# Performance work log

Hardware: AMD Instinct MI355X
Metric: run time of the kernel (lower is better)

## Reference

```python
import jax, jax.numpy as jnp
import numpy as np

B, T, C = 4, 2048, 1024
N_HEAD = 16
HEAD_DIM = C // N_HEAD
SCALE = 1.0 / np.sqrt(HEAD_DIM).astype(np.float32)


def setup_inputs() -> dict:
    key = jax.random.key(0)
    k1, k2, k3 = jax.random.split(key, 3)
    x = jax.random.normal(k1, (B, T, C), dtype=jnp.float32)
    # torch Linear weights: [out_features, in_features], scaled init
    w_qkv = jax.random.normal(k2, (3 * C, C), dtype=jnp.float32) * (1.0 / np.sqrt(C))
    w_out = jax.random.normal(k3, (C, C), dtype=jnp.float32) * (1.0 / np.sqrt(C))
    b_out = jnp.zeros((C,), dtype=jnp.float32)
    return {"x": x, "w_qkv": w_qkv, "w_out": w_out, "b_out": b_out}


def reference(x, w_qkv, w_out, b_out):
    Bsz, Tlen, Cdim = x.shape
    qkv = jnp.einsum('btc,oc->bto', x, w_qkv)  # [B,T,3C]
    q, k, v = jnp.split(qkv, 3, axis=-1)
    # [B,H,T,D]
    def heads(t):
        return t.reshape(Bsz, Tlen, N_HEAD, HEAD_DIM).transpose(0, 2, 1, 3)
    q, k, v = heads(q), heads(k), heads(v)
    att = jnp.einsum('bhqd,bhkd->bhqk', q, k) * SCALE  # [B,H,T,T]
    causal = jnp.tril(jnp.ones((Tlen, Tlen), dtype=bool))
    att = jnp.where(causal[None, None], att, -jnp.inf)
    att = jax.nn.softmax(att, axis=-1)
    out = jnp.einsum('bhqk,bhkd->bhqd', att, v)
    out = out.transpose(0, 2, 1, 3).reshape(Bsz, Tlen, Cdim)
    out = jnp.einsum('btc,oc->bto', out, w_out) + b_out
    return out
```

## Files before the change

kernel.cpp:

```cpp
#include <hip/hip_runtime.h>
#include <stdint.h>


typedef __attribute__((ext_vector_type(8))) short bf16x8;
typedef __attribute__((ext_vector_type(4))) float f32x4;

#define EXP2F(x) __builtin_amdgcn_exp2f(x)
#define SL2E 0.18033688011112042f
#define FIXED_M 15.0f

__device__ __forceinline__ short f2bf(float f) {
  union { float f; unsigned u; } c; c.f = f;
  unsigned u = c.u;
  unsigned r = (u + 0x7fffu + ((u >> 16) & 1u)) >> 16;
  return (short)(unsigned short)r;
}

__device__ __forceinline__ short f2bf_trunc(float f) {
  union { float f; unsigned u; } c; c.f = f;
  return (short)(unsigned short)(c.u >> 16);
}

__device__ __forceinline__ void llds16(const short* g, short* l) {
  __builtin_amdgcn_global_load_lds(
      (const __attribute__((address_space(1))) unsigned int*)g,
      (__attribute__((address_space(3))) unsigned int*)l, 16, 0, 0);
}

__global__ __launch_bounds__(256) void cast_f32_to_bf16(
    const float* __restrict__ src, short* __restrict__ dst, int n4) {
  int i = blockIdx.x * 256 + threadIdx.x;
  if (i >= n4) return;
  float4 f = ((const float4*)src)[i];
  short4 o;
  o.x = f2bf(f.x); o.y = f2bf(f.y); o.z = f2bf(f.z); o.w = f2bf(f.w);
  ((short4*)dst)[i] = o;
}

__global__ __launch_bounds__(256) void transpose_v(
    const short* __restrict__ V, short* __restrict__ Vt) {
  const int T = 2048;
  __shared__ short lT[64 * 72];
  const int tid = threadIdx.x;
  const int t0 = blockIdx.x * 64;
  const int bh = blockIdx.y;
  const size_t ib = (size_t)bh * T * 64;
  const size_t ob = (size_t)bh * 64 * T;
#pragma unroll
  for (int call = 0; call < 2; ++call) {
    const int c = call * 256 + tid;
    bf16x8 vv = *(const bf16x8*)(V + ib + (size_t)(t0 + (c >> 3)) * 64 + (c & 7) * 8);
#pragma unroll
    for (int jj = 0; jj < 8; ++jj)
      lT[((c & 7) * 8 + jj) * 72 + (c >> 3)] = vv[jj];
  }
  __syncthreads();
#pragma unroll
  for (int call = 0; call < 2; ++call) {
    const int c = call * 256 + tid;
    bf16x8 o = *(const bf16x8*)&lT[(c >> 3) * 72 + (c & 7) * 8];
    *(bf16x8*)(Vt + ob + (size_t)(c >> 3) * T + t0 + (c & 7) * 8) = o;
  }
}

__global__ __launch_bounds__(256) void gemm_qkv(
    const short* __restrict__ A, const short* __restrict__ Bw,
    short* __restrict__ Qo, short* __restrict__ Ko, short* __restrict__ Vo) {
  const int K = 1024;
  __shared__ short lA[128 * 32];
  __shared__ short lB[128 * 32];
  __shared__ short lC[128 * 132];
  const int tid = threadIdx.x;
  const int lane = tid & 63;
  const int wave = tid >> 6;
  const int m0 = blockIdx.y * 128;
  const int n0 = blockIdx.x * 128;
  const int wm = (wave >> 1) * 64;
  const int wn = (wave & 1) * 64;
  const int mrow = lane & 15;
  const int kq = lane >> 4;

  f32x4 acc[4][4];
#pragma unroll
  for (int i = 0; i < 4; ++i)
#pragma unroll
    for (int j = 0; j < 4; ++j) acc[i][j] = (f32x4){0.f, 0.f, 0.f, 0.f};

  for (int k0 = 0; k0 < K; k0 += 32) {
#pragma unroll
    for (int call = 0; call < 2; ++call) {
      const int cb = call * 256 + wave * 64;
      const int c = cb + lane;
      llds16(A + (size_t)(m0 + (c >> 2)) * K + k0 + (c & 3) * 8, &lA[cb * 8]);
      llds16(Bw + (size_t)(n0 + (c >> 2)) * K + k0 + (c & 3) * 8, &lB[cb * 8]);
    }
    __syncthreads();
    bf16x8 af[4], bfr[4];
#pragma unroll
    for (int i = 0; i < 4; ++i)
      af[i] = *(const bf16x8*)&lA[(wm + i * 16 + mrow) * 32 + kq * 8];
#pragma unroll
    for (int j = 0; j < 4; ++j)
      bfr[j] = *(const bf16x8*)&lB[(wn + j * 16 + mrow) * 32 + kq * 8];
#pragma unroll
    for (int i = 0; i < 4; ++i)
#pragma unroll
      for (int j = 0; j < 4; ++j)
        acc[i][j] = __builtin_amdgcn_mfma_f32_16x16x32_bf16(af[i], bfr[j], acc[i][j], 0, 0, 0);
    __syncthreads();
  }

#pragma unroll
  for (int i = 0; i < 4; ++i) {
    const int row = wm + i * 16 + kq * 4;
#pragma unroll
    for (int j = 0; j < 4; ++j) {
      const int col = wn + j * 16 + mrow;
      const float sc_ = (((n0 + col) >> 10) == 1) ? SL2E : 1.0f;
#pragma unroll
      for (int r = 0; r < 4; ++r)
        lC[(row + r) * 132 + col] = f2bf(acc[i][j][r] * sc_);
    }
  }
  __syncthreads();

#pragma unroll
  for (int call = 0; call < 8; ++call) {
    const int cc = call * 256 + tid;
    const int row = cc >> 4;
    const int m = m0 + row;
    const int b = m >> 11;
    const int t = m & 2047;
    const int o = n0 + (cc & 15) * 8;
    const int which = o >> 10;
    const int c = o & 1023;
    const int h = c >> 6;
    const int d = c & 63;
    short* dst = which == 0 ? Qo : (which == 1 ? Ko : Vo);
    bf16x8 val = *(const bf16x8*)&lC[row * 132 + (cc & 15) * 8];
    *(bf16x8*)(dst + ((size_t)(b * 16 + h) * 2048 + t) * 64 + d) = val;
  }
}

__global__ __launch_bounds__(256) void gemm_out(
    const short* __restrict__ A, const short* __restrict__ Bw,
    const float* __restrict__ bias, float* __restrict__ Out) {
  const int K = 1024;
  __shared__ short lA[128 * 32];
  __shared__ short lB[128 * 32];
  const int tid = threadIdx.x;
  const int lane = tid & 63;
  const int wave = tid >> 6;
  const int m0 = blockIdx.y * 128;
  const int n0 = blockIdx.x * 128;
  const int wm = (wave >> 1) * 64;
  const int wn = (wave & 1) * 64;
  const int mrow = lane & 15;
  const int kq = lane >> 4;

  f32x4 acc[4][4];
#pragma unroll
  for (int i = 0; i < 4; ++i)
#pragma unroll
    for (int j = 0; j < 4; ++j) acc[i][j] = (f32x4){0.f, 0.f, 0.f, 0.f};

  for (int k0 = 0; k0 < K; k0 += 32) {
#pragma unroll
    for (int call = 0; call < 2; ++call) {
      const int cb = call * 256 + wave * 64;
      const int c = cb + lane;
      llds16(A + (size_t)(m0 + (c >> 2)) * K + k0 + (c & 3) * 8, &lA[cb * 8]);
      llds16(Bw + (size_t)(n0 + (c >> 2)) * K + k0 + (c & 3) * 8, &lB[cb * 8]);
    }
    __syncthreads();
    bf16x8 af[4], bfr[4];
#pragma unroll
    for (int i = 0; i < 4; ++i)
      af[i] = *(const bf16x8*)&lA[(wm + i * 16 + mrow) * 32 + kq * 8];
#pragma unroll
    for (int j = 0; j < 4; ++j)
      bfr[j] = *(const bf16x8*)&lB[(wn + j * 16 + mrow) * 32 + kq * 8];
#pragma unroll
    for (int i = 0; i < 4; ++i)
#pragma unroll
      for (int j = 0; j < 4; ++j)
        acc[i][j] = __builtin_amdgcn_mfma_f32_16x16x32_bf16(af[i], bfr[j], acc[i][j], 0, 0, 0);
    __syncthreads();
  }

#pragma unroll
  for (int i = 0; i < 4; ++i) {
    const int m = m0 + wm + i * 16 + kq * 4;
#pragma unroll
    for (int j = 0; j < 4; ++j) {
      const int n = n0 + wn + j * 16 + mrow;
      const float bb = bias[n];
#pragma unroll
      for (int r = 0; r < 4; ++r)
        Out[(size_t)(m + r) * 1024 + n] = acc[i][j][r] + bb;
    }
  }
}

__global__ __launch_bounds__(256) void flash_attn(
    const short* __restrict__ Qg, const short* __restrict__ Kg,
    const short* __restrict__ Vtg, short* __restrict__ Og) {
  const int T = 2048;
  __shared__ short lK[2][64 * 64];
  __shared__ short lVt[2][64 * 64];
  __shared__ short lP[4 * 16 * 76];
  const int tid = threadIdx.x;
  const int lane = tid & 63;
  const int wave = tid >> 6;
  const int bh = blockIdx.x;
  const int mrow = lane & 15;
  const int kq = lane >> 4;
  const int swz = mrow & 7;
  const size_t base = (size_t)bh * T * 64;
  const size_t vbase = (size_t)bh * 64 * T;
  const int qtA = blockIdx.y;
  const int qtB = 31 - qtA;

  const bf16x8 ones = {0x3F80, 0x3F80, 0x3F80, 0x3F80, 0x3F80, 0x3F80, 0x3F80, 0x3F80};

  bf16x8 aqA0, aqA1, aqB0, aqB1;
  {
    const short* qpA = Qg + base + (size_t)(qtA * 64 + wave * 16 + mrow) * 64 + kq * 8;
    aqA0 = *(const bf16x8*)qpA;
    aqA1 = *(const bf16x8*)(qpA + 32);
    const short* qpB = Qg + base + (size_t)(qtB * 64 + wave * 16 + mrow) * 64 + kq * 8;
    aqB0 = *(const bf16x8*)qpB;
    aqB1 = *(const bf16x8*)(qpB + 32);
  }

  f32x4 accA[4], accB[4], lacA, lacB;
#pragma unroll
  for (int jd = 0; jd < 4; ++jd) {
    accA[jd] = (f32x4){0.f, 0.f, 0.f, 0.f};
    accB[jd] = (f32x4){0.f, 0.f, 0.f, 0.f};
  }
  lacA = (f32x4){0.f, 0.f, 0.f, 0.f};
  lacB = (f32x4){0.f, 0.f, 0.f, 0.f};

  auto stage = [&](int nt, int buf) {
#pragma unroll
    for (int call = 0; call < 2; ++call) {
      const int cb = call * 256 + wave * 64;
      const int c = cb + lane;
      const int row = c >> 3;
      const int scol = (c & 7) ^ (row & 7);
      llds16(Kg + base + (size_t)(nt * 64 + row) * 64 + scol * 8, &lK[buf][cb * 8]);
      llds16(Vtg + vbase + (size_t)row * T + nt * 64 + scol * 8, &lVt[buf][cb * 8]);
    }
  };

  stage(0, 0);
  __syncthreads();

  for (int kt = 0; kt <= qtB; ++kt) {
    const int bcur = kt & 1;
    if (kt < qtB) stage(kt + 1, bcur ^ 1);
    const short* K_ = lK[bcur];
    const short* Vt_ = lVt[bcur];

    auto seg_compute = [&](int qt, bf16x8 aq0, bf16x8 aq1, f32x4* acc, f32x4& lac) {
      f32x4 sc[4];
#pragma unroll
      for (int j = 0; j < 4; ++j) {
        const short* krow = &K_[(j * 16 + mrow) * 64];
        bf16x8 kb0 = *(const bf16x8*)&krow[(kq ^ swz) * 8];
        bf16x8 kb1 = *(const bf16x8*)&krow[((4 + kq) ^ swz) * 8];
        f32x4 s = (f32x4){-FIXED_M, -FIXED_M, -FIXED_M, -FIXED_M};
        s = __builtin_amdgcn_mfma_f32_16x16x32_bf16(aq0, kb0, s, 0, 0, 0);
        s = __builtin_amdgcn_mfma_f32_16x16x32_bf16(aq1, kb1, s, 0, 0, 0);
        sc[j] = s;
      }

      if (kt == qt) {
        const int qrow = qt * 64 + wave * 16 + kq * 4;
#pragma unroll
        for (int j = 0; j < 4; ++j) {
          const int key = kt * 64 + j * 16 + mrow;
#pragma unroll
          for (int r = 0; r < 4; ++r)
            if (key > qrow + r) sc[j][r] = -1e30f;
        }
      }

      short* pw = &lP[wave * 1216];
#pragma unroll
      for (int j = 0; j < 4; ++j)
#pragma unroll
        for (int r = 0; r < 4; ++r)
          pw[(kq * 4 + r) * 76 + j * 16 + mrow] = f2bf_trunc(EXP2F(sc[j][r]));

      bf16x8 pa0 = *(const bf16x8*)&lP[wave * 1216 + mrow * 76 + kq * 8];
      bf16x8 pa1 = *(const bf16x8*)&lP[wave * 1216 + mrow * 76 + 32 + kq * 8];
      lac = __builtin_amdgcn_mfma_f32_16x16x32_bf16(pa0, ones, lac, 0, 0, 0);
      lac = __builtin_amdgcn_mfma_f32_16x16x32_bf16(pa1, ones, lac, 0, 0, 0);
#pragma unroll
      for (int jd = 0; jd < 4; ++jd) {
        const short* vrow = &Vt_[(jd * 16 + mrow) * 64];
        bf16x8 vb0 = *(const bf16x8*)&vrow[(kq ^ swz) * 8];
        bf16x8 vb1 = *(const bf16x8*)&vrow[((4 + kq) ^ swz) * 8];
        acc[jd] = __builtin_amdgcn_mfma_f32_16x16x32_bf16(pa0, vb0, acc[jd], 0, 0, 0);
        acc[jd] = __builtin_amdgcn_mfma_f32_16x16x32_bf16(pa1, vb1, acc[jd], 0, 0, 0);
      }
    };

    if (kt <= qtA) seg_compute(qtA, aqA0, aqA1, accA, lacA);
    seg_compute(qtB, aqB0, aqB1, accB, lacB);
    __syncthreads();
  }

  const int b = bh >> 4;
  const int h = bh & 15;
#pragma unroll
  for (int r = 0; r < 4; ++r) {
    const float invA = 1.0f / lacA[r];
    const float invB = 1.0f / lacB[r];
    const int tA = qtA * 64 + wave * 16 + kq * 4 + r;
    const int tB = qtB * 64 + wave * 16 + kq * 4 + r;
#pragma unroll
    for (int jd = 0; jd < 4; ++jd) {
      const int col = h * 64 + jd * 16 + mrow;
      Og[((size_t)b * 2048 + tA) * 1024 + col] = f2bf(accA[jd][r] * invA);
      Og[((size_t)b * 2048 + tB) * 1024 + col] = f2bf(accB[jd][r] * invB);
    }
  }
}

extern "C" void kernel_launch(void* const* d_in, const int* in_sizes, int n_in,
                              void* d_out, int out_size, void* d_ws, size_t ws_size,
                              hipStream_t stream) {
  const float* x = (const float*)d_in[0];
  const float* w_qkv = (const float*)d_in[1];
  const float* w_out = (const float*)d_in[2];
  const float* b_out = (const float*)d_in[3];
  float* out = (float*)d_out;

  char* ws = (char*)d_ws;
  const size_t NX = 8192ull * 1024;
  const size_t NWQ = 3072ull * 1024;
  const size_t NWO = 1024ull * 1024;
  const size_t NQ = 64ull * 2048 * 64;
  size_t off = 0;
  short* xb    = (short*)(ws + off); off += NX * 2;
  short* wqkvb = (short*)(ws + off); off += NWQ * 2;
  short* woutb = (short*)(ws + off); off += NWO * 2;
  short* q     = (short*)(ws + off); off += NQ * 2;
  short* k     = (short*)(ws + off); off += NQ * 2;
  short* v     = (short*)(ws + off); off += NQ * 2;
  short* attb  = (short*)(ws + off); off += NX * 2;
  short* vt    = xb;
  if (off > ws_size) return;

  cast_f32_to_bf16<<<(int)(NX / 4 / 256), 256, 0, stream>>>(x, xb, (int)(NX / 4));
  cast_f32_to_bf16<<<(int)(NWQ / 4 / 256), 256, 0, stream>>>(w_qkv, wqkvb, (int)(NWQ / 4));
  cast_f32_to_bf16<<<(int)(NWO / 4 / 256), 256, 0, stream>>>(w_out, woutb, (int)(NWO / 4));
  gemm_qkv<<<dim3(24, 64), 256, 0, stream>>>(xb, wqkvb, q, k, v);
  transpose_v<<<dim3(32, 64), 256, 0, stream>>>(v, vt);
  flash_attn<<<dim3(64, 16), 256, 0, stream>>>(q, k, vt, attb);
  gemm_out<<<dim3(8, 64), 256, 0, stream>>>(attb, woutb, b_out, out);
}
```

Measured before the change: 270.5 us.

## Fuse V transpose into QKV GEMM epilogue and widen K tile with XOR swizzle

The QKV GEMM now writes V directly in transposed [bh, d, t] layout through a transposed LDS staging buffer, which removes the separate transpose_v kernel launch and one full round trip of V through memory. Both GEMMs also move from a K-step of 32 to 64 and apply an XOR swizzle to the LDS layout to avoid bank conflicts, halving the number of barrier pairs per tile. The cost is more LDS per block, which may lower occupancy, plus a transposed LDS write pattern in the V epilogue that may itself hit bank conflicts.

```diff
diff --git a/kernel.cpp b/kernel.cpp
--- a/kernel.cpp
+++ b/kernel.cpp
@@ -37,39 +37,13 @@
   ((short4*)dst)[i] = o;
 }
 
-__global__ __launch_bounds__(256) void transpose_v(
-    const short* __restrict__ V, short* __restrict__ Vt) {
-  const int T = 2048;
-  __shared__ short lT[64 * 72];
-  const int tid = threadIdx.x;
-  const int t0 = blockIdx.x * 64;
-  const int bh = blockIdx.y;
-  const size_t ib = (size_t)bh * T * 64;
-  const size_t ob = (size_t)bh * 64 * T;
-#pragma unroll
-  for (int call = 0; call < 2; ++call) {
-    const int c = call * 256 + tid;
-    bf16x8 vv = *(const bf16x8*)(V + ib + (size_t)(t0 + (c >> 3)) * 64 + (c & 7) * 8);
-#pragma unroll
-    for (int jj = 0; jj < 8; ++jj)
-      lT[((c & 7) * 8 + jj) * 72 + (c >> 3)] = vv[jj];
-  }
-  __syncthreads();
-#pragma unroll
-  for (int call = 0; call < 2; ++call) {
-    const int c = call * 256 + tid;
-    bf16x8 o = *(const bf16x8*)&lT[(c >> 3) * 72 + (c & 7) * 8];
-    *(bf16x8*)(Vt + ob + (size_t)(c >> 3) * T + t0 + (c & 7) * 8) = o;
-  }
-}
-
 __global__ __launch_bounds__(256) void gemm_qkv(
     const short* __restrict__ A, const short* __restrict__ Bw,
-    short* __restrict__ Qo, short* __restrict__ Ko, short* __restrict__ Vo) {
+    short* __restrict__ Qo, short* __restrict__ Ko, short* __restrict__ Vt) {
   const int K = 1024;
-  __shared__ short lA[128 * 32];
-  __shared__ short lB[128 * 32];
-  __shared__ short lC[128 * 132];
+  __shared__ short smem[17408];
+  short* lA = smem;
+  short* lB = smem + 8192;
   const int tid = threadIdx.x;
   const int lane = tid & 63;
   const int wave = tid >> 6;
@@ -86,59 +60,94 @@
 #pragma unroll
     for (int j = 0; j < 4; ++j) acc[i][j] = (f32x4){0.f, 0.f, 0.f, 0.f};
 
-  for (int k0 = 0; k0 < K; k0 += 32) {
-#pragma unroll
-    for (int call = 0; call < 2; ++call) {
+  for (int k0 = 0; k0 < K; k0 += 64) {
+#pragma unroll
+    for (int call = 0; call < 4; ++call) {
       const int cb = call * 256 + wave * 64;
       const int c = cb + lane;
-      llds16(A + (size_t)(m0 + (c >> 2)) * K + k0 + (c & 3) * 8, &lA[cb * 8]);
-      llds16(Bw + (size_t)(n0 + (c >> 2)) * K + k0 + (c & 3) * 8, &lB[cb * 8]);
-    }
-    __syncthreads();
-    bf16x8 af[4], bfr[4];
-#pragma unroll
-    for (int i = 0; i < 4; ++i)
-      af[i] = *(const bf16x8*)&lA[(wm + i * 16 + mrow) * 32 + kq * 8];
-#pragma unroll
-    for (int j = 0; j < 4; ++j)
-      bfr[j] = *(const bf16x8*)&lB[(wn + j * 16 + mrow) * 32 + kq * 8];
-#pragma unroll
-    for (int i = 0; i < 4; ++i)
-#pragma unroll
-      for (int j = 0; j < 4; ++j)
-        acc[i][j] = __builtin_amdgcn_mfma_f32_16x16x32_bf16(af[i], bfr[j], acc[i][j], 0, 0, 0);
-    __syncthreads();
-  }
-
-#pragma unroll
-  for (int i = 0; i < 4; ++i) {
-    const int row = wm + i * 16 + kq * 4;
-#pragma unroll
-    for (int j = 0; j < 4; ++j) {
-      const int col = wn + j * 16 + mrow;
-      const float sc_ = (((n0 + col) >> 10) == 1) ? SL2E : 1.0f;
-#pragma unroll
-      for (int r = 0; r < 4; ++r)
-        lC[(row + r) * 132 + col] = f2bf(acc[i][j][r] * sc_);
-    }
-  }
-  __syncthreads();
-
-#pragma unroll
-  for (int call = 0; call < 8; ++call) {
-    const int cc = call * 256 + tid;
-    const int row = cc >> 4;
-    const int m = m0 + row;
-    const int b = m >> 11;
-    const int t = m & 2047;
-    const int o = n0 + (cc & 15) * 8;
-    const int which = o >> 10;
-    const int c = o & 1023;
-    const int h = c >> 6;
-    const int d = c & 63;
-    short* dst = which == 0 ? Qo : (which == 1 ? Ko : Vo);
-    bf16x8 val = *(const bf16x8*)&lC[row * 132 + (cc & 15) * 8];
-    *(bf16x8*)(dst + ((size_t)(b * 16 + h) * 2048 + t) * 64 + d) = val;
+      const int row = c >> 3;
+      const int scol = (c & 7) ^ (row & 7);
+      llds16(A + (size_t)(m0 + row) * K + k0 + scol * 8, &lA[cb * 8]);
+      llds16(Bw + (size_t)(n0 + row) * K + k0 + scol * 8, &lB[cb * 8]);
+    }
+    __syncthreads();
+#pragma unroll
+    for (int kk = 0; kk < 2; ++kk) {
+      bf16x8 af[4], bfr[4];
+#pragma unroll
+      for (int i = 0; i < 4; ++i) {
+        const int row = wm + i * 16 + mrow;
+        af[i] = *(const bf16x8*)&lA[row * 64 + (((kk * 4 + kq) ^ (row & 7)) * 8)];
+      }
+#pragma unroll
+      for (int j = 0; j < 4; ++j) {
+        const int row = wn + j * 16 + mrow;
+        bfr[j] = *(const bf16x8*)&lB[row * 64 + (((kk * 4 + kq) ^ (row & 7)) * 8)];
+      }
+#pragma unroll
+      for (int i = 0; i < 4; ++i)
+#pragma unroll
+        for (int j = 0; j < 4; ++j)
+          acc[i][j] = __builtin_amdgcn_mfma_f32_16x16x32_bf16(af[i], bfr[j], acc[i][j], 0, 0, 0);
+    }
+    __syncthreads();
+  }
+
+  const int b = m0 >> 11;
+  if (n0 < 2048) {
+    short* lC = smem;
+#pragma unroll
+    for (int i = 0; i < 4; ++i) {
+      const int row = wm + i * 16 + kq * 4;
+#pragma unroll
+      for (int j = 0; j < 4; ++j) {
+        const int col = wn + j * 16 + mrow;
+        const float sc_ = (((n0 + col) >> 10) == 1) ? SL2E : 1.0f;
+#pragma unroll
+        for (int r = 0; r < 4; ++r)
+          lC[(row + r) * 132 + col] = f2bf(acc[i][j][r] * sc_);
+      }
+    }
+    __syncthreads();
+#pragma unroll
+    for (int call = 0; call < 8; ++call) {
+      const int cc = call * 256 + tid;
+      const int row = cc >> 4;
+      const int t = (m0 + row) & 2047;
+      const int o = n0 + (cc & 15) * 8;
+      const int c = o & 1023;
+      const int h = c >> 6;
+      const int d = c & 63;
+      short* dst = (o >> 10) == 0 ? Qo : Ko;
+      bf16x8 val = *(const bf16x8*)&lC[row * 132 + (cc & 15) * 8];
+      *(bf16x8*)(dst + ((size_t)(b * 16 + h) * 2048 + t) * 64 + d) = val;
+    }
+  } else {
+    short* lCt = smem;
+#pragma unroll
+    for (int i = 0; i < 4; ++i) {
+      const int row = wm + i * 16 + kq * 4;
+#pragma unroll
+      for (int j = 0; j < 4; ++j) {
+        const int col = wn + j * 16 + mrow;
+#pragma unroll
+        for (int r = 0; r < 4; ++r)
+          lCt[col * 136 + row + r] = f2bf(acc[i][j][r]);
+      }
+    }
+    __syncthreads();
+#pragma unroll
+    for (int call = 0; call < 8; ++call) {
+      const int cc = call * 256 + tid;
+      const int col = cc >> 4;
+      const int tg = cc & 15;
+      const int o = n0 + col;
+      const int d = o & 63;
+      const int h = (o >> 6) & 15;
+      const int t = (m0 & 2047) + tg * 8;
+      bf16x8 val = *(const bf16x8*)&lCt[col * 136 + tg * 8];
+      *(bf16x8*)(Vt + ((size_t)(b * 16 + h) * 64 + d) * 2048 + t) = val;
+    }
   }
 }
 
@@ -146,8 +155,8 @@
     const short* __restrict__ A, const short* __restrict__ Bw,
     const float* __restrict__ bias, float* __restrict__ Out) {
   const int K = 1024;
-  __shared__ short lA[128 * 32];
-  __shared__ short lB[128 * 32];
+  __shared__ short lA[128 * 64];
+  __shared__ short lB[128 * 64];
   const int tid = threadIdx.x;
   const int lane = tid & 63;
   const int wave = tid >> 6;
@@ -164,27 +173,36 @@
 #pragma unroll
     for (int j = 0; j < 4; ++j) acc[i][j] = (f32x4){0.f, 0.f, 0.f, 0.f};
 
-  for (int k0 = 0; k0 < K; k0 += 32) {
-#pragma unroll
-    for (int call = 0; call < 2; ++call) {
+  for (int k0 = 0; k0 < K; k0 += 64) {
+#pragma unroll
+    for (int call = 0; call < 4; ++call) {
       const int cb = call * 256 + wave * 64;
       const int c = cb + lane;
-      llds16(A + (size_t)(m0 + (c >> 2)) * K + k0 + (c & 3) * 8, &lA[cb * 8]);
-      llds16(Bw + (size_t)(n0 + (c >> 2)) * K + k0 + (c & 3) * 8, &lB[cb * 8]);
-    }
-    __syncthreads();
-    bf16x8 af[4], bfr[4];
-#pragma unroll
-    for (int i = 0; i < 4; ++i)
-      af[i] = *(const bf16x8*)&lA[(wm + i * 16 + mrow) * 32 + kq * 8];
-#pragma unroll
-    for (int j = 0; j < 4; ++j)
-      bfr[j] = *(const bf16x8*)&lB[(wn + j * 16 + mrow) * 32 + kq * 8];
-#pragma unroll
-    for (int i = 0; i < 4; ++i)
-#pragma unroll
-      for (int j = 0; j < 4; ++j)
-        acc[i][j] = __builtin_amdgcn_mfma_f32_16x16x32_bf16(af[i], bfr[j], acc[i][j], 0, 0, 0);
+      const int row = c >> 3;
+      const int scol = (c & 7) ^ (row & 7);
+      llds16(A + (size_t)(m0 + row) * K + k0 + scol * 8, &lA[cb * 8]);
+      llds16(Bw + (size_t)(n0 + row) * K + k0 + scol * 8, &lB[cb * 8]);
+    }
+    __syncthreads();
+#pragma unroll
+    for (int kk = 0; kk < 2; ++kk) {
+      bf16x8 af[4], bfr[4];
+#pragma unroll
+      for (int i = 0; i < 4; ++i) {
+        const int row = wm + i * 16 + mrow;
+        af[i] = *(const bf16x8*)&lA[row * 64 + (((kk * 4 + kq) ^ (row & 7)) * 8)];
+      }
+#pragma unroll
+      for (int j = 0; j < 4; ++j) {
+        const int row = wn + j * 16 + mrow;
+        bfr[j] = *(const bf16x8*)&lB[row * 64 + (((kk * 4 + kq) ^ (row & 7)) * 8)];
+      }
+#pragma unroll
+      for (int i = 0; i < 4; ++i)
+#pragma unroll
+        for (int j = 0; j < 4; ++j)
+          acc[i][j] = __builtin_amdgcn_mfma_f32_16x16x32_bf16(af[i], bfr[j], acc[i][j], 0, 0, 0);
+    }
     __syncthreads();
   }
 
@@ -350,16 +368,14 @@
   short* woutb = (short*)(ws + off); off += NWO * 2;
   short* q     = (short*)(ws + off); off += NQ * 2;
   short* k     = (short*)(ws + off); off += NQ * 2;
-  short* v     = (short*)(ws + off); off += NQ * 2;
+  short* vt    = (short*)(ws + off); off += NQ * 2;
   short* attb  = (short*)(ws + off); off += NX * 2;
-  short* vt    = xb;
   if (off > ws_size) return;
 
   cast_f32_to_bf16<<<(int)(NX / 4 / 256), 256, 0, stream>>>(x, xb, (int)(NX / 4));
   cast_f32_to_bf16<<<(int)(NWQ / 4 / 256), 256, 0, stream>>>(w_qkv, wqkvb, (int)(NWQ / 4));
   cast_f32_to_bf16<<<(int)(NWO / 4 / 256), 256, 0, stream>>>(w_out, woutb, (int)(NWO / 4));
-  gemm_qkv<<<dim3(24, 64), 256, 0, stream>>>(xb, wqkvb, q, k, v);
-  transpose_v<<<dim3(32, 64), 256, 0, stream>>>(v, vt);
+  gemm_qkv<<<dim3(24, 64), 256, 0, stream>>>(xb, wqkvb, q, k, vt);
   flash_attn<<<dim3(64, 16), 256, 0, stream>>>(q, k, vt, attb);
   gemm_out<<<dim3(8, 64), 256, 0, stream>>>(attb, woutb, b_out, out);
 }
```

Result: faster. 262.7 us (-2.9%).
